# Kernel tuning notes

Hardware: AMD Instinct MI355X
Metric: run time of the kernel (lower is better)

Reference implementation:

```python
import jax, jax.numpy as jnp
import numpy as np

V, D, H, F, L, SMAX = 32000, 768, 12, 3072, 6, 512
DN = D // H
NEG = -1e9
EPS = 1e-5


def _pos_encoding(S, d, dtype):
    # pe[pos,2i]   = sin(pos / 10000**(2i/d))
    # pe[pos,2i+1] = cos(pos / 10000**(2(i+1)/d))   (note the i+1, as in source)
    pos = jnp.arange(S, dtype=jnp.float32)[:, None]
    i = jnp.arange(d // 2, dtype=jnp.float32)[None, :]
    pe_sin = jnp.sin(pos / jnp.power(10000.0, 2.0 * i / d))
    pe_cos = jnp.cos(pos / jnp.power(10000.0, 2.0 * (i + 1.0) / d))
    pe = jnp.zeros((S, d), jnp.float32)
    pe = pe.at[:, 0::2].set(pe_sin).at[:, 1::2].set(pe_cos)
    return pe.astype(dtype)


def _layernorm(z, g, b):
    m = jnp.mean(z, axis=-1, keepdims=True)
    v = jnp.mean(jnp.square(z - m), axis=-1, keepdims=True)
    return (z - m) * jax.lax.rsqrt(v + EPS) * g + b


def setup_inputs() -> dict:
    key = jax.random.key(0)
    ks = jax.random.split(key, 20)
    s = 0.02
    inp = {
        "x": jax.random.randint(ks[0], (16, 512), 0, V, dtype=jnp.int64 if jax.config.read("jax_enable_x64") else jnp.int32),
        "padding_mask": jax.random.randint(ks[1], (16, 512, 512), 0, 2, dtype=jnp.int32),
        "emb": jax.random.normal(ks[2], (V, D), jnp.float32) * s,
        # per-head separate projections, stacked: [L, H, D, DN]
        "Wq": jax.random.normal(ks[3], (L, H, D, DN), jnp.float32) * s,
        "bq": jnp.zeros((L, H, DN), jnp.float32),
        "Wk": jax.random.normal(ks[4], (L, H, D, DN), jnp.float32) * s,
        "bk": jnp.zeros((L, H, DN), jnp.float32),
        "Wv": jax.random.normal(ks[5], (L, H, D, DN), jnp.float32) * s,
        "bv": jnp.zeros((L, H, DN), jnp.float32),
        "Wo": jax.random.normal(ks[6], (L, D, D), jnp.float32) * s,
        "bo": jnp.zeros((L, D), jnp.float32),
        "W1": jax.random.normal(ks[7], (L, D, F), jnp.float32) * s,
        "b1": jnp.zeros((L, F), jnp.float32),
        "W2": jax.random.normal(ks[8], (L, F, D), jnp.float32) * s,
        "b2": jnp.zeros((L, D), jnp.float32),
        "g1": jnp.ones((L, D), jnp.float32),
        "be1": jnp.zeros((L, D), jnp.float32),
        "g2": jnp.ones((L, D), jnp.float32),
        "be2": jnp.zeros((L, D), jnp.float32),
    }
    return inp


def reference(x, padding_mask, emb, Wq, bq, Wk, bk, Wv, bv, Wo, bo,
              W1, b1, W2, b2, g1, be1, g2, be2):
    B, S = x.shape
    h = emb[x]                                   # [B,S,D]
    h = h + _pos_encoding(S, D, h.dtype)[None]   # dropout is identity in eval
    bias = padding_mask.astype(h.dtype)[:, None] * NEG   # [B,1,S,S]
    scale = 1.0 / np.sqrt(DN)
    for l in range(L):
        q = jnp.einsum("bsd,hde->bhse", h, Wq[l]) + bq[l][None, :, None, :]
        k = jnp.einsum("bsd,hde->bhse", h, Wk[l]) + bk[l][None, :, None, :]
        v = jnp.einsum("bsd,hde->bhse", h, Wv[l]) + bv[l][None, :, None, :]
        scores = jnp.einsum("bhse,bhte->bhst", q, k) * scale + bias
        attn = jax.nn.softmax(scores, axis=-1)
        o = jnp.einsum("bhst,bhte->bhse", attn, v)        # [B,H,S,DN]
        o = o.transpose(0, 2, 1, 3).reshape(B, S, D)      # concat heads
        o = o @ Wo[l] + bo[l]
        h = _layernorm(h + o, g1[l], be1[l])
        ff = jax.nn.relu(h @ W1[l] + b1[l]) @ W2[l] + b2[l]
        h = _layernorm(h + ff, g2[l], be2[l])
    return h
```

## Files before the change

kernel.cpp:

```cpp
#include <hip/hip_runtime.h>
#include <hip/hip_bf16.h>
#include <math.h>

#define B_  16
#define S_  512
#define D_  768
#define H_  12
#define DN_ 64
#define F_  3072
#define L_  6
#define T_  (B_*S_)
#define QKVN 2304

typedef unsigned short ushort_t;
typedef short short8 __attribute__((ext_vector_type(8)));
typedef float floatx4 __attribute__((ext_vector_type(4)));

#define LDS_AS(p) ((__attribute__((address_space(3))) void*)(p))
#define GLB_AS(p) ((const __attribute__((address_space(1))) void*)(p))

static __device__ __forceinline__ float b2f(ushort_t u) {
  union { unsigned int i; float f; } x; x.i = ((unsigned int)u) << 16; return x.f;
}
static __device__ __forceinline__ ushort_t f2b(float f) {
  union { float f; unsigned int i; } x; x.f = f;
  unsigned int r = x.i + 0x7fffu + ((x.i >> 16) & 1u);
  return (ushort_t)(r >> 16);
}

__global__ __launch_bounds__(64) void probe_x(const int* __restrict__ x,
                                              int* __restrict__ xstride) {
  if (threadIdx.x == 0) {
    int allzero = 1;
    for (int i = 0; i < 64; ++i) allzero &= (x[2 * i + 1] == 0) ? 1 : 0;
    *xstride = allzero ? 2 : 1;
  }
}

__global__ __launch_bounds__(256) void embed_pe(const int* __restrict__ x,
                                                const int* __restrict__ xstride,
                                                const float* __restrict__ emb,
                                                float* __restrict__ h32,
                                                ushort_t* __restrict__ h16) {
  const int t = blockIdx.x;
  const int s = t & (S_ - 1);
  const int tok = x[t * (*xstride)];
  const float* ep = emb + (size_t)tok * D_;
  const float pos = (float)s;
  for (int d = threadIdx.x; d < D_; d += 256) {
    float pe;
    if ((d & 1) == 0) {
      float freq = powf(10000.0f, -(float)d * (1.0f / 768.0f));
      pe = sinf(pos * freq);
    } else {
      float freq = powf(10000.0f, -(float)(d + 1) * (1.0f / 768.0f));
      pe = cosf(pos * freq);
    }
    float v = ep[d] + pe;
    h32[(size_t)t * D_ + d] = v;
    h16[(size_t)t * D_ + d] = f2b(v);
  }
}

__global__ __launch_bounds__(256) void mask_bias(const int* __restrict__ mask,
                                                 ushort_t* __restrict__ bias) {
  const size_t i = ((size_t)blockIdx.x * 256 + threadIdx.x) * 4;
  int4 m = *(const int4*)(mask + i);
  ushort4 o;
  o.x = m.x ? f2b(-1e9f) : (ushort_t)0;
  o.y = m.y ? f2b(-1e9f) : (ushort_t)0;
  o.z = m.z ? f2b(-1e9f) : (ushort_t)0;
  o.w = m.w ? f2b(-1e9f) : (ushort_t)0;
  *(ushort4*)(bias + i) = o;
}

__global__ __launch_bounds__(256) void pack_bias(const float* __restrict__ bq,
                                                 const float* __restrict__ bk,
                                                 const float* __restrict__ bv,
                                                 float* __restrict__ bqkv) {
  const int i = blockIdx.x * 256 + threadIdx.x;
  if (i < L_ * D_) {
    const int l = i / D_, c = i - l * D_;
    bqkv[(size_t)l * QKVN + c]          = bq[i];
    bqkv[(size_t)l * QKVN + 768 + c]    = bk[i];
    bqkv[(size_t)l * QKVN + 1536 + c]   = bv[i];
  }
}

__global__ __launch_bounds__(256) void transpose_cast(const float* __restrict__ in,
                                                      ushort_t* __restrict__ out,
                                                      int R, int C, int ZH,
                                                      size_t strideL, size_t strideH) {
  __shared__ float tb[32][33];
  const int c0 = blockIdx.x * 32, r0 = blockIdx.y * 32;
  const int z = blockIdx.z;
  const float* ib = in + (size_t)z * R * C;
  ushort_t* ob = out + (size_t)(z / ZH) * strideL + (size_t)(z % ZH) * strideH;
  const int i = threadIdx.x >> 5;
  const int j = threadIdx.x & 31;
  #pragma unroll
  for (int t = 0; t < 4; ++t)
    tb[i + 8 * t][j] = ib[(size_t)(r0 + i + 8 * t) * C + c0 + j];
  __syncthreads();
  #pragma unroll
  for (int t = 0; t < 4; ++t)
    ob[(size_t)(c0 + i + 8 * t) * R + r0 + j] = f2b(tb[j][i + 8 * t]);
}

__global__ __launch_bounds__(256) void transpose_v(const ushort_t* __restrict__ qkv,
                                                   ushort_t* __restrict__ vT) {
  __shared__ ushort_t tb[32][33];
  const int s0 = blockIdx.x * 32, e0 = blockIdx.y * 32;
  const int bh = blockIdx.z;
  const int b = bh / 12, hh = bh - b * 12;
  const int i = threadIdx.x >> 5, j = threadIdx.x & 31;
  #pragma unroll
  for (int t = 0; t < 4; ++t)
    tb[i + 8 * t][j] = qkv[((size_t)(b * S_ + s0 + i + 8 * t)) * QKVN + 1536 + hh * 64 + e0 + j];
  __syncthreads();
  #pragma unroll
  for (int t = 0; t < 4; ++t)
    vT[((size_t)(bh * 64 + e0 + i + 8 * t)) * S_ + s0 + j] = tb[j][i + 8 * t];
}

template<int RELU>
__global__ __launch_bounds__(256) void gemm_mfma(const ushort_t* __restrict__ A,
                                                 const ushort_t* __restrict__ Bt,
                                                 const float* __restrict__ bias,
                                                 ushort_t* __restrict__ C,
                                                 int N, int K) {
  __shared__ ushort_t Alds[128 * 32];
  __shared__ ushort_t Blds[128 * 32];
  const int tid = threadIdx.x;
  const int lane = tid & 63, wave = tid >> 6;
  const int l16 = lane & 15, quad = lane >> 4;
  const int m0 = (wave >> 1) * 64, n0 = (wave & 1) * 64;
  const int nb = gridDim.x;
  const int flat = blockIdx.y * nb + blockIdx.x;
  const int grp = flat / (8 * nb);
  const int rem = flat - grp * 8 * nb;
  const int bm = (grp * 8 + (rem & 7)) * 128;
  const int bn = (rem >> 3) * 128;
  const int r0 = tid >> 2, koff = (tid & 3) * 8;

  const ushort_t* ga0 = A  + (size_t)(bm + r0) * K + koff;
  const ushort_t* ga1 = ga0 + (size_t)64 * K;
  const ushort_t* gb0 = Bt + (size_t)(bn + r0) * K + koff;
  const ushort_t* gb1 = gb0 + (size_t)64 * K;
  ushort_t* la0 = &Alds[tid * 8];
  ushort_t* la1 = &Alds[64 * 32 + tid * 8];
  ushort_t* lb0 = &Blds[tid * 8];
  ushort_t* lb1 = &Blds[64 * 32 + tid * 8];

  floatx4 acc[4][4] = {};
  for (int k0 = 0; k0 < K; k0 += 32) {
    __syncthreads();
    __builtin_amdgcn_global_load_lds(GLB_AS(ga0 + k0), LDS_AS(la0), 16, 0, 0);
    __builtin_amdgcn_global_load_lds(GLB_AS(ga1 + k0), LDS_AS(la1), 16, 0, 0);
    __builtin_amdgcn_global_load_lds(GLB_AS(gb0 + k0), LDS_AS(lb0), 16, 0, 0);
    __builtin_amdgcn_global_load_lds(GLB_AS(gb1 + k0), LDS_AS(lb1), 16, 0, 0);
    __syncthreads();
    short8 af[4], bf[4];
    #pragma unroll
    for (int fi = 0; fi < 4; ++fi)
      af[fi] = *(const short8*)&Alds[(m0 + fi * 16 + l16) * 32 + quad * 8];
    #pragma unroll
    for (int fj = 0; fj < 4; ++fj)
      bf[fj] = *(const short8*)&Blds[(n0 + fj * 16 + l16) * 32 + quad * 8];
    #pragma unroll
    for (int fi = 0; fi < 4; ++fi)
      #pragma unroll
      for (int fj = 0; fj < 4; ++fj)
        acc[fi][fj] = __builtin_amdgcn_mfma_f32_16x16x32_bf16(af[fi], bf[fj], acc[fi][fj], 0, 0, 0);
  }
  #pragma unroll
  for (int fi = 0; fi < 4; ++fi) {
    #pragma unroll
    for (int fj = 0; fj < 4; ++fj) {
      const int row = bm + m0 + fi * 16 + quad * 4;
      const int col = bn + n0 + fj * 16 + l16;
      const float bv = bias[col];
      #pragma unroll
      for (int r = 0; r < 4; ++r) {
        float v = acc[fi][fj][r] + bv;
        if (RELU) v = fmaxf(v, 0.0f);
        C[(size_t)(row + r) * N + col] = f2b(v);
      }
    }
  }
}

__global__ __launch_bounds__(256) void attn_mfma(const ushort_t* __restrict__ qkv,
                                                 const ushort_t* __restrict__ vT,
                                                 const ushort_t* __restrict__ bias,
                                                 ushort_t* __restrict__ o) {
  __shared__ ushort_t Qs[64][72];
  __shared__ ushort_t Ks[64][72];
  __shared__ ushort_t Vt[64][72];
  __shared__ ushort_t Ps[64][72];
  const int qt = blockIdx.x, hh = blockIdx.y, b = blockIdx.z;
  const int tid = threadIdx.x;
  const int lane = tid & 63, w = tid >> 6;
  const int l16 = lane & 15, quad = lane >> 4;

  for (int c = tid; c < 1024; c += 256) {
    const int row = c >> 4, e0 = (c & 15) * 4;
    *(ushort4*)&Qs[row][e0] =
        *(const ushort4*)(qkv + ((size_t)(b * S_ + qt * 64 + row)) * QKVN + hh * 64 + e0);
  }

  floatx4 Oa[4] = {};
  float mrow[4] = {-3e38f, -3e38f, -3e38f, -3e38f};
  float lrow[4] = {};
  const ushort_t* vbase = vT + ((size_t)(b * H_ + hh) * 64) * S_;

  for (int kt = 0; kt < 8; ++kt) {
    __syncthreads();
    for (int c = tid; c < 1024; c += 256) {
      const int row = c >> 4, e0 = (c & 15) * 4;
      *(ushort4*)&Ks[row][e0] =
          *(const ushort4*)(qkv + ((size_t)(b * S_ + kt * 64 + row)) * QKVN + 768 + hh * 64 + e0);
      *(ushort4*)&Vt[row][e0] =
          *(const ushort4*)(vbase + (size_t)row * S_ + kt * 64 + e0);
    }
    __syncthreads();

    floatx4 sa[4] = {};
    #pragma unroll
    for (int st = 0; st < 2; ++st) {
      short8 aq = *(const short8*)&Qs[w * 16 + l16][st * 32 + quad * 8];
      #pragma unroll
      for (int fj = 0; fj < 4; ++fj) {
        short8 bk = *(const short8*)&Ks[fj * 16 + l16][st * 32 + quad * 8];
        sa[fj] = __builtin_amdgcn_mfma_f32_16x16x32_bf16(aq, bk, sa[fj], 0, 0, 0);
      }
    }

    #pragma unroll
    for (int r = 0; r < 4; ++r) {
      const int qrow = qt * 64 + w * 16 + quad * 4 + r;
      const ushort_t* bp = bias + ((size_t)b * S_ + qrow) * S_ + kt * 64 + l16;
      float s0 = sa[0][r] * 0.125f + b2f(bp[0]);
      float s1 = sa[1][r] * 0.125f + b2f(bp[16]);
      float s2 = sa[2][r] * 0.125f + b2f(bp[32]);
      float s3 = sa[3][r] * 0.125f + b2f(bp[48]);
      float mt = fmaxf(fmaxf(s0, s1), fmaxf(s2, s3));
      mt = fmaxf(mt, __shfl_xor(mt, 1)); mt = fmaxf(mt, __shfl_xor(mt, 2));
      mt = fmaxf(mt, __shfl_xor(mt, 4)); mt = fmaxf(mt, __shfl_xor(mt, 8));
      const float mn = fmaxf(mrow[r], mt);
      const float alpha = __expf(mrow[r] - mn);
      mrow[r] = mn;
      float p0 = __expf(s0 - mn), p1 = __expf(s1 - mn);
      float p2 = __expf(s2 - mn), p3 = __expf(s3 - mn);
      const int prow = w * 16 + quad * 4 + r;
      Ps[prow][ 0 + l16] = f2b(p0);
      Ps[prow][16 + l16] = f2b(p1);
      Ps[prow][32 + l16] = f2b(p2);
      Ps[prow][48 + l16] = f2b(p3);
      float rs = p0 + p1 + p2 + p3;
      rs += __shfl_xor(rs, 1); rs += __shfl_xor(rs, 2);
      rs += __shfl_xor(rs, 4); rs += __shfl_xor(rs, 8);
      lrow[r] = lrow[r] * alpha + rs;
      Oa[0][r] *= alpha; Oa[1][r] *= alpha; Oa[2][r] *= alpha; Oa[3][r] *= alpha;
    }

    #pragma unroll
    for (int st = 0; st < 2; ++st) {
      short8 ap = *(const short8*)&Ps[w * 16 + l16][st * 32 + quad * 8];
      #pragma unroll
      for (int fe = 0; fe < 4; ++fe) {
        short8 bv = *(const short8*)&Vt[fe * 16 + l16][st * 32 + quad * 8];
        Oa[fe] = __builtin_amdgcn_mfma_f32_16x16x32_bf16(ap, bv, Oa[fe], 0, 0, 0);
      }
    }
  }

  #pragma unroll
  for (int r = 0; r < 4; ++r) {
    const float inv = 1.0f / lrow[r];
    const size_t tok = (size_t)(b * S_ + qt * 64 + w * 16 + quad * 4 + r);
    #pragma unroll
    for (int fe = 0; fe < 4; ++fe)
      o[tok * D_ + hh * 64 + fe * 16 + l16] = f2b(Oa[fe][r] * inv);
  }
}

__global__ __launch_bounds__(256) void add_ln(float* __restrict__ h,
                                              const ushort_t* __restrict__ r,
                                              const float* __restrict__ g,
                                              const float* __restrict__ be,
                                              ushort_t* __restrict__ h16) {
  const int t = blockIdx.x;
  const int tid = threadIdx.x;
  __shared__ float red[8];
  const size_t base = (size_t)t * D_;
  float x0 = h[base + tid]       + b2f(r[base + tid]);
  float x1 = h[base + tid + 256] + b2f(r[base + tid + 256]);
  float x2 = h[base + tid + 512] + b2f(r[base + tid + 512]);
  float s = x0 + x1 + x2;
  #pragma unroll
  for (int off = 32; off > 0; off >>= 1) s += __shfl_down(s, off);
  if ((tid & 63) == 0) red[tid >> 6] = s;
  __syncthreads();
  if (tid == 0) red[4] = (red[0] + red[1] + red[2] + red[3]) * (1.0f / 768.0f);
  __syncthreads();
  const float m = red[4];
  float d0 = x0 - m, d1 = x1 - m, d2 = x2 - m;
  float s2 = d0 * d0 + d1 * d1 + d2 * d2;
  #pragma unroll
  for (int off = 32; off > 0; off >>= 1) s2 += __shfl_down(s2, off);
  if ((tid & 63) == 0) red[tid >> 6] = s2;
  __syncthreads();
  if (tid == 0) red[5] = (red[0] + red[1] + red[2] + red[3]) * (1.0f / 768.0f);
  __syncthreads();
  const float rs = rsqrtf(red[5] + 1e-5f);
  float y0 = d0 * rs * g[tid]       + be[tid];
  float y1 = d1 * rs * g[tid + 256] + be[tid + 256];
  float y2 = d2 * rs * g[tid + 512] + be[tid + 512];
  h[base + tid]       = y0; h16[base + tid]       = f2b(y0);
  h[base + tid + 256] = y1; h16[base + tid + 256] = f2b(y1);
  h[base + tid + 512] = y2; h16[base + tid + 512] = f2b(y2);
}

__global__ __launch_bounds__(256) void write_out(const float* __restrict__ h,
                                                 float* __restrict__ out, int n) {
  int i = blockIdx.x * 256 + threadIdx.x;
  if (i < n) out[i] = h[i];
}

extern "C" void kernel_launch(void* const* d_in, const int* in_sizes, int n_in,
                              void* d_out, int out_size, void* d_ws, size_t ws_size,
                              hipStream_t stream) {
  (void)in_sizes; (void)n_in; (void)out_size; (void)ws_size;
  const int* x    = (const int*)d_in[0];
  const int* mask = (const int*)d_in[1];
  const float* emb = (const float*)d_in[2];
  const float* Wq  = (const float*)d_in[3];
  const float* bq  = (const float*)d_in[4];
  const float* Wk  = (const float*)d_in[5];
  const float* bk  = (const float*)d_in[6];
  const float* Wv  = (const float*)d_in[7];
  const float* bv  = (const float*)d_in[8];
  const float* Wo  = (const float*)d_in[9];
  const float* bo  = (const float*)d_in[10];
  const float* W1  = (const float*)d_in[11];
  const float* b1  = (const float*)d_in[12];
  const float* W2  = (const float*)d_in[13];
  const float* b2  = (const float*)d_in[14];
  const float* g1  = (const float*)d_in[15];
  const float* be1 = (const float*)d_in[16];
  const float* g2  = (const float*)d_in[17];
  const float* be2 = (const float*)d_in[18];

  const size_t TD  = (size_t)T_ * D_;
  const size_t DD  = (size_t)D_ * D_;
  const size_t WDD = (size_t)L_ * DD;
  const size_t WDF = (size_t)L_ * D_ * F_;

  float* h32 = (float*)d_ws;
  ushort_t* h16  = (ushort_t*)(h32 + TD);
  ushort_t* qkv16 = h16 + TD;
  ushort_t* o1   = qkv16 + 3 * TD;
  ushort_t* o2   = o1 + TD;
  ushort_t* ff   = qkv16;
  ushort_t* vT   = o2 + TD;
  ushort_t* bias16 = vT + TD;
  ushort_t* WqkvT = bias16 + (size_t)B_ * S_ * S_;
  ushort_t* WoT  = WqkvT + 3 * WDD;
  ushort_t* W1T  = WoT + WDD;
  ushort_t* W2T  = W1T + WDF;
  float* bqkv    = (float*)(W2T + WDF);
  int* xstride   = (int*)(bqkv + (size_t)L_ * QKVN);

  probe_x<<<dim3(1), 64, 0, stream>>>(x, xstride);
  transpose_cast<<<dim3(2, 24, 72), 256, 0, stream>>>(Wq, WqkvT,          768, 64, 12, 3 * DD, (size_t)64 * 768);
  transpose_cast<<<dim3(2, 24, 72), 256, 0, stream>>>(Wk, WqkvT + DD,     768, 64, 12, 3 * DD, (size_t)64 * 768);
  transpose_cast<<<dim3(2, 24, 72), 256, 0, stream>>>(Wv, WqkvT + 2 * DD, 768, 64, 12, 3 * DD, (size_t)64 * 768);
  transpose_cast<<<dim3(24, 24, 6), 256, 0, stream>>>(Wo, WoT, 768, 768, 1, DD, 0);
  transpose_cast<<<dim3(96, 24, 6), 256, 0, stream>>>(W1, W1T, 768, 3072, 1, (size_t)D_ * F_, 0);
  transpose_cast<<<dim3(24, 96, 6), 256, 0, stream>>>(W2, W2T, 3072, 768, 1, (size_t)D_ * F_, 0);
  pack_bias<<<dim3((L_ * D_ + 255) / 256), 256, 0, stream>>>(bq, bk, bv, bqkv);
  mask_bias<<<dim3((B_ * S_ * S_) / 1024), 256, 0, stream>>>(mask, bias16);
  embed_pe<<<dim3(T_), 256, 0, stream>>>(x, xstride, emb, h32, h16);

  const dim3 gQKV(QKVN / 128, T_ / 128);
  const dim3 gD(D_ / 128, T_ / 128);
  const dim3 gF(F_ / 128, T_ / 128);
  for (int l = 0; l < L_; ++l) {
    const size_t oDD = (size_t)l * DD;
    const size_t oDF = (size_t)l * D_ * F_;
    gemm_mfma<0><<<gQKV, 256, 0, stream>>>(h16, WqkvT + (size_t)l * 3 * DD, bqkv + (size_t)l * QKVN, qkv16, QKVN, D_);
    transpose_v<<<dim3(16, 2, B_ * H_), 256, 0, stream>>>(qkv16, vT);
    attn_mfma<<<dim3(8, H_, B_), 256, 0, stream>>>(qkv16, vT, bias16, o1);
    gemm_mfma<0><<<gD, 256, 0, stream>>>(o1, WoT + oDD, bo + l * D_, o2, D_, D_);
    add_ln<<<dim3(T_), 256, 0, stream>>>(h32, o2, g1 + l * D_, be1 + l * D_, h16);
    gemm_mfma<1><<<gF, 256, 0, stream>>>(h16, W1T + oDF, b1 + l * F_, ff, F_, D_);
    gemm_mfma<0><<<gD, 256, 0, stream>>>(ff, W2T + oDF, b2 + l * D_, o2, D_, F_);
    add_ln<<<dim3(T_), 256, 0, stream>>>(h32, o2, g2 + l * D_, be2 + l * D_, h16);
  }
  write_out<<<dim3((unsigned)(TD / 256)), 256, 0, stream>>>(h32, (float*)d_out, (int)TD);
}
```

Before: 2.150 ms.

## Split-K the D-output GEMMs and fold partial sums into add_ln

Adds a split-K variant of the MFMA GEMM for the Wo and W2 projections, whose output width is 768. Each projection now launches twice as many blocks, with each block covering half of K. The two bf16 partial outputs are written to adjacent buffers, and the residual add-layernorm kernel sums them. This is meant to improve load balance across CUs for the narrow-N GEMMs, at the cost of extra output traffic and an extra rounding of the partials to bf16. Separately, the positional encoding is precomputed once into a scratch buffer, so the embedding kernel no longer runs sin/cos/pow per token.

After: 1.998 ms. -7.1%, faster.

```diff
diff --git a/kernel.cpp b/kernel.cpp
--- a/kernel.cpp
+++ b/kernel.cpp
@@ -11,6 +11,7 @@
 #define L_  6
 #define T_  (B_*S_)
 #define QKVN 2304
+#define TDC ((size_t)T_*D_)
 
 typedef unsigned short ushort_t;
 typedef short short8 __attribute__((ext_vector_type(8)));
@@ -37,26 +38,35 @@
   }
 }
 
+__global__ __launch_bounds__(256) void pe_kernel(float* __restrict__ pe) {
+  const int s = blockIdx.x;
+  const float pos = (float)s;
+  for (int d = threadIdx.x; d < D_; d += 256) {
+    float v;
+    if ((d & 1) == 0) {
+      float freq = powf(10000.0f, -(float)d * (1.0f / 768.0f));
+      v = sinf(pos * freq);
+    } else {
+      float freq = powf(10000.0f, -(float)(d + 1) * (1.0f / 768.0f));
+      v = cosf(pos * freq);
+    }
+    pe[(size_t)s * D_ + d] = v;
+  }
+}
+
 __global__ __launch_bounds__(256) void embed_pe(const int* __restrict__ x,
                                                 const int* __restrict__ xstride,
                                                 const float* __restrict__ emb,
+                                                const float* __restrict__ pe,
                                                 float* __restrict__ h32,
                                                 ushort_t* __restrict__ h16) {
   const int t = blockIdx.x;
   const int s = t & (S_ - 1);
   const int tok = x[t * (*xstride)];
   const float* ep = emb + (size_t)tok * D_;
-  const float pos = (float)s;
+  const float* pp = pe + (size_t)s * D_;
   for (int d = threadIdx.x; d < D_; d += 256) {
-    float pe;
-    if ((d & 1) == 0) {
-      float freq = powf(10000.0f, -(float)d * (1.0f / 768.0f));
-      pe = sinf(pos * freq);
-    } else {
-      float freq = powf(10000.0f, -(float)(d + 1) * (1.0f / 768.0f));
-      pe = cosf(pos * freq);
-    }
-    float v = ep[d] + pe;
+    float v = ep[d] + pp[d];
     h32[(size_t)t * D_ + d] = v;
     h16[(size_t)t * D_ + d] = f2b(v);
   }
@@ -185,6 +195,74 @@
         float v = acc[fi][fj][r] + bv;
         if (RELU) v = fmaxf(v, 0.0f);
         C[(size_t)(row + r) * N + col] = f2b(v);
+      }
+    }
+  }
+}
+
+__global__ __launch_bounds__(256) void gemm_mfma_sk(const ushort_t* __restrict__ A,
+                                                    const ushort_t* __restrict__ Bt,
+                                                    const float* __restrict__ bias,
+                                                    ushort_t* __restrict__ P,
+                                                    int N, int K) {
+  __shared__ ushort_t Alds[128 * 32];
+  __shared__ ushort_t Blds[128 * 32];
+  const int tid = threadIdx.x;
+  const int lane = tid & 63, wave = tid >> 6;
+  const int l16 = lane & 15, quad = lane >> 4;
+  const int m0 = (wave >> 1) * 64, n0 = (wave & 1) * 64;
+  const int nb = gridDim.x;
+  const int flat = blockIdx.y * nb + blockIdx.x;
+  const int grp = flat / (8 * nb);
+  const int rem = flat - grp * 8 * nb;
+  const int bm = (grp * 8 + (rem & 7)) * 128;
+  const int bn = (rem >> 3) * 128;
+  const int r0 = tid >> 2, koff = (tid & 3) * 8;
+  const int z = blockIdx.z;
+  const int Kh = K >> 1;
+
+  const ushort_t* ga0 = A  + (size_t)(bm + r0) * K + (size_t)z * Kh + koff;
+  const ushort_t* ga1 = ga0 + (size_t)64 * K;
+  const ushort_t* gb0 = Bt + (size_t)(bn + r0) * K + (size_t)z * Kh + koff;
+  const ushort_t* gb1 = gb0 + (size_t)64 * K;
+  ushort_t* la0 = &Alds[tid * 8];
+  ushort_t* la1 = &Alds[64 * 32 + tid * 8];
+  ushort_t* lb0 = &Blds[tid * 8];
+  ushort_t* lb1 = &Blds[64 * 32 + tid * 8];
+  ushort_t* Pz = P + (size_t)z * T_ * N;
+
+  floatx4 acc[4][4] = {};
+  for (int k0 = 0; k0 < Kh; k0 += 32) {
+    __syncthreads();
+    __builtin_amdgcn_global_load_lds(GLB_AS(ga0 + k0), LDS_AS(la0), 16, 0, 0);
+    __builtin_amdgcn_global_load_lds(GLB_AS(ga1 + k0), LDS_AS(la1), 16, 0, 0);
+    __builtin_amdgcn_global_load_lds(GLB_AS(gb0 + k0), LDS_AS(lb0), 16, 0, 0);
+    __builtin_amdgcn_global_load_lds(GLB_AS(gb1 + k0), LDS_AS(lb1), 16, 0, 0);
+    __syncthreads();
+    short8 af[4], bf[4];
+    #pragma unroll
+    for (int fi = 0; fi < 4; ++fi)
+      af[fi] = *(const short8*)&Alds[(m0 + fi * 16 + l16) * 32 + quad * 8];
+    #pragma unroll
+    for (int fj = 0; fj < 4; ++fj)
+      bf[fj] = *(const short8*)&Blds[(n0 + fj * 16 + l16) * 32 + quad * 8];
+    #pragma unroll
+    for (int fi = 0; fi < 4; ++fi)
+      #pragma unroll
+      for (int fj = 0; fj < 4; ++fj)
+        acc[fi][fj] = __builtin_amdgcn_mfma_f32_16x16x32_bf16(af[fi], bf[fj], acc[fi][fj], 0, 0, 0);
+  }
+  #pragma unroll
+  for (int fi = 0; fi < 4; ++fi) {
+    #pragma unroll
+    for (int fj = 0; fj < 4; ++fj) {
+      const int row = bm + m0 + fi * 16 + quad * 4;
+      const int col = bn + n0 + fj * 16 + l16;
+      const float bv = (z == 0) ? bias[col] : 0.0f;
+      #pragma unroll
+      for (int r = 0; r < 4; ++r) {
+        float v = acc[fi][fj][r] + bv;
+        Pz[(size_t)(row + r) * N + col] = f2b(v);
       }
     }
   }
@@ -294,9 +372,9 @@
   const int tid = threadIdx.x;
   __shared__ float red[8];
   const size_t base = (size_t)t * D_;
-  float x0 = h[base + tid]       + b2f(r[base + tid]);
-  float x1 = h[base + tid + 256] + b2f(r[base + tid + 256]);
-  float x2 = h[base + tid + 512] + b2f(r[base + tid + 512]);
+  float x0 = h[base + tid]       + b2f(r[base + tid])       + b2f(r[TDC + base + tid]);
+  float x1 = h[base + tid + 256] + b2f(r[base + tid + 256]) + b2f(r[TDC + base + tid + 256]);
+  float x2 = h[base + tid + 512] + b2f(r[base + tid + 512]) + b2f(r[TDC + base + tid + 512]);
   float s = x0 + x1 + x2;
   #pragma unroll
   for (int off = 32; off > 0; off >>= 1) s += __shfl_down(s, off);
@@ -352,7 +430,7 @@
   const float* g2  = (const float*)d_in[17];
   const float* be2 = (const float*)d_in[18];
 
-  const size_t TD  = (size_t)T_ * D_;
+  const size_t TD  = TDC;
   const size_t DD  = (size_t)D_ * D_;
   const size_t WDD = (size_t)L_ * DD;
   const size_t WDF = (size_t)L_ * D_ * F_;
@@ -371,8 +449,10 @@
   ushort_t* W2T  = W1T + WDF;
   float* bqkv    = (float*)(W2T + WDF);
   int* xstride   = (int*)(bqkv + (size_t)L_ * QKVN);
+  float* pe32    = (float*)o1;
 
   probe_x<<<dim3(1), 64, 0, stream>>>(x, xstride);
+  pe_kernel<<<dim3(S_), 256, 0, stream>>>(pe32);
   transpose_cast<<<dim3(2, 24, 72), 256, 0, stream>>>(Wq, WqkvT,          768, 64, 12, 3 * DD, (size_t)64 * 768);
   transpose_cast<<<dim3(2, 24, 72), 256, 0, stream>>>(Wk, WqkvT + DD,     768, 64, 12, 3 * DD, (size_t)64 * 768);
   transpose_cast<<<dim3(2, 24, 72), 256, 0, stream>>>(Wv, WqkvT + 2 * DD, 768, 64, 12, 3 * DD, (size_t)64 * 768);
@@ -381,10 +461,10 @@
   transpose_cast<<<dim3(24, 96, 6), 256, 0, stream>>>(W2, W2T, 3072, 768, 1, (size_t)D_ * F_, 0);
   pack_bias<<<dim3((L_ * D_ + 255) / 256), 256, 0, stream>>>(bq, bk, bv, bqkv);
   mask_bias<<<dim3((B_ * S_ * S_) / 1024), 256, 0, stream>>>(mask, bias16);
-  embed_pe<<<dim3(T_), 256, 0, stream>>>(x, xstride, emb, h32, h16);
+  embed_pe<<<dim3(T_), 256, 0, stream>>>(x, xstride, emb, pe32, h32, h16);
 
   const dim3 gQKV(QKVN / 128, T_ / 128);
-  const dim3 gD(D_ / 128, T_ / 128);
+  const dim3 gDsk(D_ / 128, T_ / 128, 2);
   const dim3 gF(F_ / 128, T_ / 128);
   for (int l = 0; l < L_; ++l) {
     const size_t oDD = (size_t)l * DD;
@@ -392,10 +472,10 @@
     gemm_mfma<0><<<gQKV, 256, 0, stream>>>(h16, WqkvT + (size_t)l * 3 * DD, bqkv + (size_t)l * QKVN, qkv16, QKVN, D_);
     transpose_v<<<dim3(16, 2, B_ * H_), 256, 0, stream>>>(qkv16, vT);
     attn_mfma<<<dim3(8, H_, B_), 256, 0, stream>>>(qkv16, vT, bias16, o1);
-    gemm_mfma<0><<<gD, 256, 0, stream>>>(o1, WoT + oDD, bo + l * D_, o2, D_, D_);
+    gemm_mfma_sk<<<gDsk, 256, 0, stream>>>(o1, WoT + oDD, bo + l * D_, o2, D_, D_);
     add_ln<<<dim3(T_), 256, 0, stream>>>(h32, o2, g1 + l * D_, be1 + l * D_, h16);
     gemm_mfma<1><<<gF, 256, 0, stream>>>(h16, W1T + oDF, b1 + l * F_, ff, F_, D_);
-    gemm_mfma<0><<<gD, 256, 0, stream>>>(ff, W2T + oDF, b2 + l * D_, o2, D_, F_);
+    gemm_mfma_sk<<<gDsk, 256, 0, stream>>>(ff, W2T + oDF, b2 + l * D_, o2, D_, F_);
     add_ln<<<dim3(T_), 256, 0, stream>>>(h32, o2, g2 + l * D_, be2 + l * D_, h16);
   }
   write_out<<<dim3((unsigned)(TD / 256)), 256, 0, stream>>>(h32, (float*)d_out, (int)TD);
```
